# Performance work log

Measured on AMD Instinct MI355X. Metric: run time of the kernel, lower is better.

Reference implementation:

```python
import jax, jax.numpy as jnp
import numpy as np

INPUT_SIZE = 64
HIDDEN_SIZE = 128
LATENT_B = 8
BATCH = 512
SEQ = 2048


def setup_inputs() -> dict:
    key = jax.random.key(0)
    ks = jax.random.split(key, 8)
    s_fc = 1.0 / np.sqrt(INPUT_SIZE)
    s_gru = 1.0 / np.sqrt(LATENT_B)
    return {
        "latent_A_seq": jax.random.normal(ks[0], (BATCH, SEQ, INPUT_SIZE), dtype=jnp.float32),
        # fc_in: Linear(input_size -> hidden_size)
        "W_in": jax.random.uniform(ks[1], (HIDDEN_SIZE, INPUT_SIZE), jnp.float32, -s_fc, s_fc),
        "b_in": jax.random.uniform(ks[2], (HIDDEN_SIZE,), jnp.float32, -s_fc, s_fc),
        # GRU(hidden_size -> latent_dim_B), PyTorch layout: [3*H, in] stacked as (r, z, n)
        "W_ih": jax.random.uniform(ks[3], (3 * LATENT_B, HIDDEN_SIZE), jnp.float32, -s_gru, s_gru),
        "W_hh": jax.random.uniform(ks[4], (3 * LATENT_B, LATENT_B), jnp.float32, -s_gru, s_gru),
        "b_ih": jax.random.uniform(ks[5], (3 * LATENT_B,), jnp.float32, -s_gru, s_gru),
        "b_hh": jax.random.uniform(ks[6], (3 * LATENT_B,), jnp.float32, -s_gru, s_gru),
    }


def reference(latent_A_seq, W_in, b_in, W_ih, W_hh, b_ih, b_hh):
    # fc_in projection: (B, S, input) -> (B, S, hidden)
    x = jnp.einsum("bsi,hi->bsh", latent_A_seq, W_in) + b_in
    H = W_hh.shape[1]

    # Precompute input-side gate activations for all timesteps: (B, S, 3H)
    x_gates = jnp.einsum("bsh,gh->bsg", x, W_ih) + b_ih
    xr, xz, xn = jnp.split(x_gates, 3, axis=-1)

    Whr, Whz, Whn = jnp.split(W_hh, 3, axis=0)
    bhr, bhz, bhn = jnp.split(b_hh, 3, axis=0)

    def step(h, gates_t):
        xr_t, xz_t, xn_t = gates_t
        r = jax.nn.sigmoid(xr_t + h @ Whr.T + bhr)
        z = jax.nn.sigmoid(xz_t + h @ Whz.T + bhz)
        n = jnp.tanh(xn_t + r * (h @ Whn.T + bhn))
        h_new = (1.0 - z) * n + z * h
        return h_new, None

    h0 = jnp.zeros((latent_A_seq.shape[0], H), dtype=latent_A_seq.dtype)
    # scan over time: move seq axis to front -> (S, B, H) per gate
    seq_gates = (jnp.swapaxes(xr, 0, 1), jnp.swapaxes(xz, 0, 1), jnp.swapaxes(xn, 0, 1))
    h_final, _ = jax.lax.scan(step, h0, seq_gates)
    return h_final  # (B, latent_dim_B) == h_n.squeeze(0)
```

## Files before the change

### kernel.cpp

```cpp
#include <hip/hip_runtime.h>
#include <math.h>

#define BATCH  512
#define SEQ    2048
#define INPUT  64
#define HID    128
#define LB     8
#define NG     24
#define T      16
#define NCHUNK (SEQ / T)
#define SLABF  (LB * NG)
#define CH_F   (T * SLABF)
#define ROWS   (T * LB)
#define AF4C   (ROWS * 16)

#define LOG2E  1.44269504088896340736f

typedef float v2f __attribute__((ext_vector_type(2)));

__device__ __forceinline__ v2f mk2(float a, float b) { v2f r; r.x = a; r.y = b; return r; }

#if __has_builtin(__builtin_amdgcn_exp2f)
#define EXP2F(x) __builtin_amdgcn_exp2f(x)
#else
#define EXP2F(x) __expf(0.69314718055994530942f * (x))
#endif

__global__ void precompute_kernel(const float* __restrict__ W_in,
                                  const float* __restrict__ b_in,
                                  const float* __restrict__ W_ih,
                                  const float* __restrict__ b_ih,
                                  const float* __restrict__ b_hh,
                                  float* __restrict__ Wc,
                                  float* __restrict__ bc)
{
    int t = blockIdx.x * blockDim.x + threadIdx.x;
    if (t < NG * INPUT) {
        int g = t / INPUT, i = t % INPUT;
        float acc = 0.f;
        for (int h = 0; h < HID; ++h)
            acc += W_ih[g * HID + h] * W_in[h * INPUT + i];
        float sc = (g < 2 * LB) ? -LOG2E : 2.0f * LOG2E;
        Wc[t] = acc * sc;
    } else if (t < NG * INPUT + NG) {
        int g = t - NG * INPUT;
        float acc = b_ih[g];
        if (g < 2 * LB) acc += b_hh[g];
        for (int h = 0; h < HID; ++h)
            acc += W_ih[g * HID + h] * b_in[h];
        float sc = (g < 2 * LB) ? -LOG2E : 2.0f * LOG2E;
        bc[g] = acc * sc;
    }
}

#define ROR2(v)  __int_as_float(__builtin_amdgcn_update_dpp(0, __float_as_int(v), 0x122, 0xF, 0xF, false))
#define ROR4(v)  __int_as_float(__builtin_amdgcn_update_dpp(0, __float_as_int(v), 0x124, 0xF, 0xF, false))
#define ROR8(v)  __int_as_float(__builtin_amdgcn_update_dpp(0, __float_as_int(v), 0x128, 0xF, 0xF, false))

#define GATHER8(sl, x) do {      \
    sl[0] = (x);                 \
    sl[1] = ROR2(sl[0]);         \
    sl[2] = ROR4(sl[0]);         \
    sl[3] = ROR4(sl[1]);         \
    sl[4] = ROR8(sl[0]);         \
    sl[5] = ROR8(sl[1]);         \
    sl[6] = ROR8(sl[2]);         \
    sl[7] = ROR8(sl[3]);         \
} while (0)

__global__ __launch_bounds__(256, 1) void fused_kernel(
    const float* __restrict__ A,
    const float* __restrict__ Wc,
    const float* __restrict__ bc,
    const float* __restrict__ W_hh,
    const float* __restrict__ b_hh,
    float* __restrict__ out)
{
    __shared__ float4 abuf[2][AF4C];
    __shared__ float  sbuf[2][CH_F];

    const int tid = threadIdx.x;
    const int wv  = tid >> 6;
    const int l   = tid & 63;
    const int b0  = blockIdx.x * 8;

    if (wv < 3) {
        const int pg = wv * 64 + l;
        const int gp = pg % 12;
        const int rg = pg / 12;
        const int g0 = gp * 2, g1 = g0 + 1;
        const int j0 = g0 & 7, t0 = g0 >> 3;
        const int j1 = g1 & 7, t1 = g1 >> 3;

        v2f w0l[16], w0h[16], w1l[16], w1h[16];
        const float4* W4 = (const float4*)Wc;
#pragma unroll
        for (int i = 0; i < 16; ++i) {
            float4 a = W4[g0 * 16 + i];
            float4 b = W4[g1 * 16 + i];
            w0l[i] = mk2(a.x, a.y); w0h[i] = mk2(a.z, a.w);
            w1l[i] = mk2(b.x, b.y); w1h[i] = mk2(b.z, b.w);
        }
        const float bc0 = bc[g0], bc1 = bc[g1];

        auto stage = [&](int cc) {
            float4* ab = &abuf[cc & 1][0];
            const size_t srow = (size_t)cc * T;
#pragma unroll
            for (int k = 0; k < 11; ++k) {
                int kk = k * 3 + wv;
                if (kk < 32) {
                    int q = kk * 64 + l;
                    int r = q >> 4;
                    int i = q & 15;
                    int isrc = i ^ ((r >> 3) & 7);
                    const float* gsrc = A
                        + ((size_t)(b0 + (r >> 4)) * SEQ + srow + (size_t)(r & 15)) * INPUT
                        + isrc * 4;
                    __builtin_amdgcn_global_load_lds(
                        (const __attribute__((address_space(1))) unsigned int*)gsrc,
                        (__attribute__((address_space(3))) unsigned int*)(ab + kk * 64),
                        16, 0, 0);
                }
            }
        };

        auto compute_slab = [&](int cc) {
            const float4* ab = &abuf[cc & 1][0];
            float* sl = &sbuf[cc & 1][0];
#pragma unroll
            for (int rit = 0; rit < 8; ++rit) {
                const int r  = rg * 8 + rit;
                const int xk = (r >> 3) & 7;
                const float4* arow = ab + r * 16;
                v2f acc0 = mk2(bc0, 0.f);
                v2f acc1 = mk2(bc1, 0.f);
#pragma unroll
                for (int i = 0; i < 16; ++i) {
                    float4 a4 = arow[i ^ xk];
                    v2f alo = mk2(a4.x, a4.y);
                    v2f ahi = mk2(a4.z, a4.w);
                    acc0 = acc0 + alo * w0l[i] + ahi * w0h[i];
                    acc1 = acc1 + alo * w1l[i] + ahi * w1h[i];
                }
                const int sw = r & 15, bh = r >> 4;
                float* sp = sl + sw * SLABF + bh * (LB * 3);
                sp[j0 * 3 + t0] = acc0.x + acc0.y;
                sp[j1 * 3 + t1] = acc1.x + acc1.y;
            }
        };

        stage(0);
        asm volatile("s_waitcnt vmcnt(0)" ::: "memory");
        __syncthreads();
        stage(1);
        compute_slab(0);
        asm volatile("s_waitcnt vmcnt(0)" ::: "memory");
        __syncthreads();

        for (int p = 0; p < NCHUNK; ++p) {
            if (p + 2 < NCHUNK) stage(p + 2);
            if (p + 1 < NCHUNK) {
                compute_slab(p + 1);
                asm volatile("s_waitcnt vmcnt(0)" ::: "memory");
                __syncthreads();
            }
        }
    } else {
        const int row = l >> 4;
        const int j   = (l >> 1) & 7;
        const int g   = l & 1;
        const int bh  = row * 2 + g;
        const int b   = b0 + bh;
        const int cofs = (bh * LB + j) * 3;

        float jdxv[8];
        GATHER8(jdxv, (float)j);
        float wrs[8], wzs[8], wns[8];
#pragma unroll
        for (int m = 0; m < 8; ++m) {
            int idx = (int)(jdxv[m] + 0.5f);
            wrs[m] = W_hh[(0 * LB + j) * LB + idx] * (-LOG2E);
            wzs[m] = W_hh[(1 * LB + j) * LB + idx] * (-LOG2E);
            wns[m] = W_hh[(2 * LB + j) * LB + idx] * (2.0f * LOG2E);
        }
        v2f wr2[4], wz2[4], wn2[4];
#pragma unroll
        for (int m = 0; m < 4; ++m) {
            wr2[m] = mk2(wrs[2 * m], wrs[2 * m + 1]);
            wz2[m] = mk2(wzs[2 * m], wzs[2 * m + 1]);
            wn2[m] = mk2(wns[2 * m], wns[2 * m + 1]);
        }
        const float bhn = b_hh[2 * LB + j] * (2.0f * LOG2E);

        float h = 0.f;
        __syncthreads();
        __syncthreads();

        for (int p = 0; p < NCHUNK; ++p) {
            const float* Lb = &sbuf[p & 1][cofs];

            float cr = Lb[0],         cz = Lb[1],         cn = Lb[2];
            float nr = Lb[SLABF + 0], nz = Lb[SLABF + 1], nn = Lb[SLABF + 2];
#pragma unroll
            for (int d = 0; d < T; ++d) {
                float fr = 0.f, fz = 0.f, fn = 0.f;
                if (d + 2 < T) {
                    const float* q = Lb + (d + 2) * SLABF;
                    fr = q[0]; fz = q[1]; fn = q[2];
                }

                float hs[8];
                GATHER8(hs, h);
                v2f h0 = mk2(hs[0], hs[1]);
                v2f h1 = mk2(hs[2], hs[3]);
                v2f h2 = mk2(hs[4], hs[5]);
                v2f h3 = mk2(hs[6], hs[7]);

                v2f srv = h0 * wr2[0] + h1 * wr2[1] + (h2 * wr2[2] + h3 * wr2[3]);
                v2f szv = h0 * wz2[0] + h1 * wz2[1] + (h2 * wz2[2] + h3 * wz2[3]);
                v2f snv = h0 * wn2[0] + h1 * wn2[1] + (h2 * wn2[2] + h3 * wn2[3]);

                float dr = cr + (srv.x + srv.y);
                float dz = cz + (szv.x + szv.y);
                float dn = bhn + (snv.x + snv.y);

                float er = EXP2F(dr);
                float ez = EXP2F(dz);
                float rr = __builtin_amdgcn_rcpf(1.f + er);
                float zz = __builtin_amdgcn_rcpf(1.f + ez);

                float tt = fmaf(rr, dn, cn);
                float en = EXP2F(tt);
                float nv = fmaf(-2.f, __builtin_amdgcn_rcpf(1.f + en), 1.f);

                h = fmaf(zz, h - nv, nv);

                cr = nr; cz = nz; cn = nn;
                nr = fr; nz = fz; nn = fn;
            }
            if (p + 1 < NCHUNK) __syncthreads();
        }

        out[b * LB + j] = h;
    }
}

extern "C" void kernel_launch(void* const* d_in, const int* in_sizes, int n_in,
                              void* d_out, int out_size, void* d_ws, size_t ws_size,
                              hipStream_t stream) {
    const float* A    = (const float*)d_in[0];
    const float* W_in = (const float*)d_in[1];
    const float* b_in = (const float*)d_in[2];
    const float* W_ih = (const float*)d_in[3];
    const float* W_hh = (const float*)d_in[4];
    const float* b_ih = (const float*)d_in[5];
    const float* b_hh = (const float*)d_in[6];
    float* out = (float*)d_out;

    float* Wc = (float*)d_ws;
    float* bc = Wc + NG * INPUT;

    precompute_kernel<<<7, 256, 0, stream>>>(W_in, b_in, W_ih, b_ih, b_hh, Wc, bc);
    fused_kernel<<<BATCH / 8, 256, 0, stream>>>(A, Wc, bc, W_hh, b_hh, out);
}
```

Before: 701.2 us.

## Stage A through registers and move fused weights to padded LDS

Replaces the direct global-to-LDS async loads with register-staged loads. The loads are issued before the compute and written to the alternate LDS buffer afterward, with address offsets precomputed once. The fused weight matrix moves from 64 per-thread registers into a padded LDS table. The slab compute is reordered so each weight float4 is reused across 8 rows with 16 accumulators. This frees registers and changes the memory pipeline, but adds LDS reads for weights and a register-held prefetch buffer. The write into buffer p&1 may also race with the scan warp reading the slab or abuf.

```diff
diff --git a/kernel.cpp b/kernel.cpp
--- a/kernel.cpp
+++ b/kernel.cpp
@@ -13,6 +13,7 @@
 #define CH_F   (T * SLABF)
 #define ROWS   (T * LB)
 #define AF4C   (ROWS * 16)
+#define WPAD   17
 
 #define LOG2E  1.44269504088896340736f
 
@@ -78,11 +79,18 @@
 {
     __shared__ float4 abuf[2][AF4C];
     __shared__ float  sbuf[2][CH_F];
+    __shared__ float4 wlds[NG * WPAD];
 
     const int tid = threadIdx.x;
     const int wv  = tid >> 6;
     const int l   = tid & 63;
     const int b0  = blockIdx.x * 8;
+
+    {
+        const float4* Wc4 = (const float4*)Wc;
+        for (int idx = tid; idx < NG * 16; idx += 256)
+            wlds[(idx >> 4) * WPAD + (idx & 15)] = Wc4[idx];
+    }
 
     if (wv < 3) {
         const int pg = wv * 64 + l;
@@ -91,80 +99,82 @@
         const int g0 = gp * 2, g1 = g0 + 1;
         const int j0 = g0 & 7, t0 = g0 >> 3;
         const int j1 = g1 & 7, t1 = g1 >> 3;
-
-        v2f w0l[16], w0h[16], w1l[16], w1h[16];
-        const float4* W4 = (const float4*)Wc;
-#pragma unroll
-        for (int i = 0; i < 16; ++i) {
-            float4 a = W4[g0 * 16 + i];
-            float4 b = W4[g1 * 16 + i];
-            w0l[i] = mk2(a.x, a.y); w0h[i] = mk2(a.z, a.w);
-            w1l[i] = mk2(b.x, b.y); w1h[i] = mk2(b.z, b.w);
-        }
+        const int xk = rg & 7;
         const float bc0 = bc[g0], bc1 = bc[g1];
 
-        auto stage = [&](int cc) {
-            float4* ab = &abuf[cc & 1][0];
-            const size_t srow = (size_t)cc * T;
-#pragma unroll
-            for (int k = 0; k < 11; ++k) {
-                int kk = k * 3 + wv;
-                if (kk < 32) {
-                    int q = kk * 64 + l;
-                    int r = q >> 4;
-                    int i = q & 15;
-                    int isrc = i ^ ((r >> 3) & 7);
-                    const float* gsrc = A
-                        + ((size_t)(b0 + (r >> 4)) * SEQ + srow + (size_t)(r & 15)) * INPUT
-                        + isrc * 4;
-                    __builtin_amdgcn_global_load_lds(
-                        (const __attribute__((address_space(1))) unsigned int*)gsrc,
-                        (__attribute__((address_space(3))) unsigned int*)(ab + kk * 64),
-                        16, 0, 0);
+        int goff[11], loff[11];
+#pragma unroll
+        for (int k = 0; k < 11; ++k) {
+            int kk = k * 3 + wv;
+            if (kk < 32) {
+                int q = kk * 64 + l;
+                int r = q >> 4;
+                int i = q & 15;
+                goff[k] = ((r >> 4) * SEQ + (r & 15)) * INPUT + i * 4;
+                loff[k] = r * 16 + (i ^ ((r >> 3) & 7));
+            } else { goff[k] = 0; loff[k] = 0; }
+        }
+
+        const float* gbase = A + (size_t)b0 * SEQ * INPUT;
+        float4 rq[11];
+
+        auto stage_load = [&]() {
+#pragma unroll
+            for (int k = 0; k < 11; ++k)
+                if (k * 3 + wv < 32) rq[k] = *(const float4*)(gbase + goff[k]);
+            gbase += T * INPUT;
+        };
+        auto stage_write = [&](int h) {
+            float4* ab = &abuf[h][0];
+#pragma unroll
+            for (int k = 0; k < 11; ++k)
+                if (k * 3 + wv < 32) ab[loff[k]] = rq[k];
+        };
+        auto compute_slab = [&](int h) {
+            const float4* ab = &abuf[h][0];
+            float* sl = &sbuf[h][0];
+            v2f acc0[8], acc1[8];
+#pragma unroll
+            for (int rit = 0; rit < 8; ++rit) {
+                acc0[rit] = mk2(bc0, 0.f);
+                acc1[rit] = mk2(bc1, 0.f);
+            }
+#pragma unroll
+            for (int i = 0; i < 16; ++i) {
+                float4 w0 = wlds[g0 * WPAD + i];
+                float4 w1 = wlds[g1 * WPAD + i];
+                v2f w0l = mk2(w0.x, w0.y), w0h = mk2(w0.z, w0.w);
+                v2f w1l = mk2(w1.x, w1.y), w1h = mk2(w1.z, w1.w);
+#pragma unroll
+                for (int rit = 0; rit < 8; ++rit) {
+                    float4 a4 = ab[(rg * 8 + rit) * 16 + (i ^ xk)];
+                    v2f alo = mk2(a4.x, a4.y), ahi = mk2(a4.z, a4.w);
+                    acc0[rit] += alo * w0l + ahi * w0h;
+                    acc1[rit] += alo * w1l + ahi * w1h;
                 }
             }
+#pragma unroll
+            for (int rit = 0; rit < 8; ++rit) {
+                int r = rg * 8 + rit;
+                float* sp = sl + (r & 15) * SLABF + (r >> 4) * (LB * 3);
+                sp[j0 * 3 + t0] = acc0[rit].x + acc0[rit].y;
+                sp[j1 * 3 + t1] = acc1[rit].x + acc1[rit].y;
+            }
         };
 
-        auto compute_slab = [&](int cc) {
-            const float4* ab = &abuf[cc & 1][0];
-            float* sl = &sbuf[cc & 1][0];
-#pragma unroll
-            for (int rit = 0; rit < 8; ++rit) {
-                const int r  = rg * 8 + rit;
-                const int xk = (r >> 3) & 7;
-                const float4* arow = ab + r * 16;
-                v2f acc0 = mk2(bc0, 0.f);
-                v2f acc1 = mk2(bc1, 0.f);
-#pragma unroll
-                for (int i = 0; i < 16; ++i) {
-                    float4 a4 = arow[i ^ xk];
-                    v2f alo = mk2(a4.x, a4.y);
-                    v2f ahi = mk2(a4.z, a4.w);
-                    acc0 = acc0 + alo * w0l[i] + ahi * w0h[i];
-                    acc1 = acc1 + alo * w1l[i] + ahi * w1h[i];
-                }
-                const int sw = r & 15, bh = r >> 4;
-                float* sp = sl + sw * SLABF + bh * (LB * 3);
-                sp[j0 * 3 + t0] = acc0.x + acc0.y;
-                sp[j1 * 3 + t1] = acc1.x + acc1.y;
-            }
-        };
-
-        stage(0);
-        asm volatile("s_waitcnt vmcnt(0)" ::: "memory");
-        __syncthreads();
-        stage(1);
+        stage_load();
+        stage_write(0);
+        __syncthreads();
+        stage_load();
         compute_slab(0);
-        asm volatile("s_waitcnt vmcnt(0)" ::: "memory");
+        stage_write(1);
         __syncthreads();
 
         for (int p = 0; p < NCHUNK; ++p) {
-            if (p + 2 < NCHUNK) stage(p + 2);
-            if (p + 1 < NCHUNK) {
-                compute_slab(p + 1);
-                asm volatile("s_waitcnt vmcnt(0)" ::: "memory");
-                __syncthreads();
-            }
+            if (p + 2 < NCHUNK) stage_load();
+            if (p + 1 < NCHUNK) compute_slab((p + 1) & 1);
+            if (p + 2 < NCHUNK) stage_write(p & 1);
+            if (p + 1 < NCHUNK) __syncthreads();
         }
     } else {
         const int row = l >> 4;
```

Measured after the change: 1.072 ms. +52.9%, slower.
